# Optimization experiments

Measured on AMD Instinct MI355X. Metric: run time of the kernel, lower is better.

Reference implementation:

```python
import jax, jax.numpy as jnp
import numpy as np

S, B, V, E, H, L = 500, 64, 50257, 512, 512, 2


def setup_inputs() -> dict:
    key = jax.random.key(0)
    ks = jax.random.split(key, 12)
    u = lambda k, shape, s: jax.random.uniform(k, shape, jnp.float32, -s, s)
    kstd = 1.0 / np.sqrt(H)
    return {
        "inputs": jax.random.randint(ks[0], (S, B), 0, V, dtype=jnp.int64),
        "text_lengths": jax.random.randint(ks[1], (B,), 1, S, dtype=jnp.int64),
        "embedding": jax.random.normal(ks[2], (V, E), jnp.float32),
        "W_ih": u(ks[3], (4 * H, E), kstd),   # PyTorch LSTM gate order: i,f,g,o
        "W_hh": u(ks[4], (4 * H, H), kstd),
        "b_ih": u(ks[5], (4 * H,), kstd),
        "b_hh": u(ks[6], (4 * H,), kstd),
        "W_word": u(ks[7], (H, H), 0.1),
        "b_word": jnp.zeros((H, 1), jnp.float32),
        "w_proj": u(ks[8], (H, 1), 0.1),
        "dec_W": u(ks[9], (L, H), kstd),
        "dec_b": u(ks[10], (L,), kstd),
    }


def _lstm(x, W_ih, W_hh, b_ih, b_hh):
    # x: [S, B, E] -> states [S, B, H]
    Bsz = x.shape[1]
    Hn = W_hh.shape[1]
    # precompute input projections for all timesteps in one GEMM
    xproj = jnp.einsum('sbe,ge->sbg', x, W_ih) + b_ih + b_hh  # [S, B, 4H]

    def step(carry, xp):
        h, c = carry
        z = xp + h @ W_hh.T  # [B, 4H]
        i, f, g, o = jnp.split(z, 4, axis=-1)
        i, f, o = jax.nn.sigmoid(i), jax.nn.sigmoid(f), jax.nn.sigmoid(o)
        c = f * c + i * jnp.tanh(g)
        h = o * jnp.tanh(c)
        return (h, c), h

    h0 = jnp.zeros((Bsz, Hn), x.dtype)
    _, hs = jax.lax.scan(step, (h0, h0), xproj)
    return hs  # [S, B, H]


def reference(inputs, text_lengths, embedding, W_ih, W_hh, b_ih, b_hh,
              W_word, b_word, w_proj, dec_W, dec_b):
    # eval mode: dropout is identity
    embedded = embedding[inputs]                       # [S, B, E]
    states = _lstm(embedded, W_ih, W_hh, b_ih, b_hh)   # [S, B, H]
    # batch_matmul_bias with tanh: tanh(states @ W_word + b_word^T)
    word_squish = jnp.tanh(jnp.einsum('sbh,hk->sbk', states, W_word) + b_word[:, 0])
    # batch_matmul: project to scalar score per (s, b)
    word_attn = jnp.einsum('sbh,hk->sbk', word_squish, w_proj)[..., 0]  # [S, B]
    # softmax over sequence dim (nn.Softmax on [B, S] -> dim=1)
    attn = jax.nn.softmax(word_attn.T, axis=1).T       # [S, B]
    # attention_mul: weighted sum over S, keepdim -> [1, B, H]
    pooled = jnp.einsum('sb,sbh->bh', attn, states)[None]
    return pooled @ dec_W.T + dec_b                    # [1, B, labels]
```

## Files before the change

### kernel.cpp

```cpp
#include <hip/hip_runtime.h>


#define S_LEN 500
#define BATCH 64
#define EDIM 512
#define HDIM 512
#define TEAMS 8
#define WGS_PER_TEAM 32
#define TB 8
#define NBLOCKS (TEAMS * WGS_PER_TEAM)
#define NTHREADS 512

typedef unsigned long long ull;

#define XPROJ_BYTES  ((size_t)S_LEN * 2048 * BATCH * 4)
#define STATES_OFF   XPROJ_BYTES
#define STATES_BYTES ((size_t)S_LEN * BATCH * HDIM * 4)
#define HBUF_OFF     (STATES_OFF + STATES_BYTES)
#define HBUF_BYTES   ((size_t)2 * TEAMS * TB * HDIM * 8)
#define PART_OFF     (HBUF_OFF + HBUF_BYTES)
#define PART_BYTES   (4 * S_LEN * BATCH * 4)

__global__ __launch_bounds__(256) void xproj_gemm(
    const int* __restrict__ idx, const float* __restrict__ emb,
    const float* __restrict__ W_ih, const float* __restrict__ b_ih,
    const float* __restrict__ b_hh, float* __restrict__ xproj) {
  __shared__ float At[16][132];
  __shared__ float Bt[16][132];
  __shared__ int sidx[128];

  const int tid = threadIdx.x;
  const int sb0 = blockIdx.x * 128;
  const int g0  = blockIdx.y * 128;
  if (tid < 128) sidx[tid] = idx[sb0 + tid];

  const int ty = tid >> 4, tx = tid & 15;
  const int ra = tid & 127, pp = tid >> 7;

  float acc[8][8];
#pragma unroll
  for (int i = 0; i < 8; ++i)
#pragma unroll
    for (int j = 0; j < 8; ++j) acc[i][j] = 0.f;

  __syncthreads();

  for (int k0 = 0; k0 < 512; k0 += 16) {
    const float* pa = &W_ih[(size_t)(g0 + ra) * 512 + k0 + 8 * pp];
    float4 a0 = *(const float4*)pa, a1 = *(const float4*)(pa + 4);
    const float* pb = &emb[(size_t)sidx[ra] * 512 + k0 + 8 * pp];
    float4 b0 = *(const float4*)pb, b1 = *(const float4*)(pb + 4);
    At[8*pp+0][ra]=a0.x; At[8*pp+1][ra]=a0.y; At[8*pp+2][ra]=a0.z; At[8*pp+3][ra]=a0.w;
    At[8*pp+4][ra]=a1.x; At[8*pp+5][ra]=a1.y; At[8*pp+6][ra]=a1.z; At[8*pp+7][ra]=a1.w;
    Bt[8*pp+0][ra]=b0.x; Bt[8*pp+1][ra]=b0.y; Bt[8*pp+2][ra]=b0.z; Bt[8*pp+3][ra]=b0.w;
    Bt[8*pp+4][ra]=b1.x; Bt[8*pp+5][ra]=b1.y; Bt[8*pp+6][ra]=b1.z; Bt[8*pp+7][ra]=b1.w;
    __syncthreads();
#pragma unroll
    for (int kk = 0; kk < 16; ++kk) {
      float4 x0 = *(const float4*)&At[kk][ty * 8];
      float4 x1 = *(const float4*)&At[kk][ty * 8 + 4];
      float4 y0 = *(const float4*)&Bt[kk][tx * 8];
      float4 y1 = *(const float4*)&Bt[kk][tx * 8 + 4];
      float av[8] = {x0.x, x0.y, x0.z, x0.w, x1.x, x1.y, x1.z, x1.w};
      float bv[8] = {y0.x, y0.y, y0.z, y0.w, y1.x, y1.y, y1.z, y1.w};
#pragma unroll
      for (int i = 0; i < 8; ++i)
#pragma unroll
        for (int j = 0; j < 8; ++j) acc[i][j] = fmaf(av[i], bv[j], acc[i][j]);
    }
    __syncthreads();
  }
  const int sbb = sb0 + tx * 8;
  const int s  = sbb >> 6;
  const int tm = (sbb & 63) >> 3;
#pragma unroll
  for (int i = 0; i < 8; ++i) {
    const int g = g0 + ty * 8 + i;
    const float bias = b_ih[g] + b_hh[g];
    float* dst = &xproj[(((size_t)s * TEAMS + tm) * 2048 + g) * 8];
    float4 v0 = {acc[i][0] + bias, acc[i][1] + bias, acc[i][2] + bias, acc[i][3] + bias};
    float4 v1 = {acc[i][4] + bias, acc[i][5] + bias, acc[i][6] + bias, acc[i][7] + bias};
    *(float4*)dst = v0;
    *(float4*)(dst + 4) = v1;
  }
}

__global__ __launch_bounds__(NTHREADS, 1) void lstm_persistent(
    const float* __restrict__ xproj, const float* __restrict__ W_hh,
    float* __restrict__ states, ull* __restrict__ h_buf) {
  __shared__ float red[2][8][4][65];

  const int team = blockIdx.x & 7;
  const int wg   = blockIdx.x >> 3;
  const int tid  = threadIdx.x;
  const int wv   = tid >> 6;
  const int l    = tid & 63;

  const int g = 16 * wg + (l & 15) + 512 * (l >> 4);

  float whh[64];
  {
    const float4* phh = (const float4*)(W_hh + (size_t)g * HDIM + (size_t)wv * 64);
#pragma unroll
    for (int j = 0; j < 16; ++j) {
      float4 v = phh[j];
      whh[4*j+0] = v.x; whh[4*j+1] = v.y; whh[4*j+2] = v.z; whh[4*j+3] = v.w;
    }
  }

  const int gu = l & 15, gbl = l >> 4;
  const int unit = 16 * wg + gu;
  float c_state = 0.f;
  const float* xpbase = xproj + (size_t)(16 * wg + gu) * 8 + (wv * 4 + gbl);

  for (int s = 0; s < S_LEN; ++s) {
    const int par = s & 1, par2 = (s + 1) & 1;
#pragma unroll
    for (int G = 0; G < 2; ++G) {
      float xv0, xv1, xv2, xv3;
      if (wv == G) {
        const float* p = xpbase + ((size_t)s * TEAMS + team) * (2048 * 8);
        xv0 = p[0]; xv1 = p[512 * 8]; xv2 = p[1024 * 8]; xv3 = p[1536 * 8];
      }

      float acc0 = 0.f, acc1 = 0.f, acc2 = 0.f, acc3 = 0.f;
      if (s > 0) {
        const ull* hb = h_buf + (((size_t)par * TEAMS + team) * TB + G * 4) * HDIM
                        + (size_t)64 * wv + l;
        ull r0, r1, r2, r3;
        int spins = 0;
        for (;;) {
          r0 = __hip_atomic_load(hb + 0 * HDIM, __ATOMIC_RELAXED, __HIP_MEMORY_SCOPE_AGENT);
          r1 = __hip_atomic_load(hb + 1 * HDIM, __ATOMIC_RELAXED, __HIP_MEMORY_SCOPE_AGENT);
          r2 = __hip_atomic_load(hb + 2 * HDIM, __ATOMIC_RELAXED, __HIP_MEMORY_SCOPE_AGENT);
          r3 = __hip_atomic_load(hb + 3 * HDIM, __ATOMIC_RELAXED, __HIP_MEMORY_SCOPE_AGENT);
          bool ok = ((int)(r0 >> 32) == s) & ((int)(r1 >> 32) == s) &
                    ((int)(r2 >> 32) == s) & ((int)(r3 >> 32) == s);
          if (__all(ok)) break;
          __builtin_amdgcn_s_sleep(1);
          if (++spins > (1 << 18)) break;
        }
        const int h0 = (int)(unsigned)r0, h1 = (int)(unsigned)r1;
        const int h2 = (int)(unsigned)r2, h3 = (int)(unsigned)r3;
#pragma unroll
        for (int k = 0; k < 64; ++k) {
          const float wk = whh[k];
          acc0 = fmaf(wk, __int_as_float(__builtin_amdgcn_readlane(h0, k)), acc0);
          acc1 = fmaf(wk, __int_as_float(__builtin_amdgcn_readlane(h1, k)), acc1);
          acc2 = fmaf(wk, __int_as_float(__builtin_amdgcn_readlane(h2, k)), acc2);
          acc3 = fmaf(wk, __int_as_float(__builtin_amdgcn_readlane(h3, k)), acc3);
        }
      }

      red[G][wv][0][l] = acc0;
      red[G][wv][1][l] = acc1;
      red[G][wv][2][l] = acc2;
      red[G][wv][3][l] = acc3;
      __syncthreads();

      if (wv == G) {
        float z0 = xv0, z1 = xv1, z2 = xv2, z3 = xv3;
#pragma unroll
        for (int w2 = 0; w2 < 8; ++w2) {
          z0 += red[G][w2][gbl][gu +  0];
          z1 += red[G][w2][gbl][gu + 16];
          z2 += red[G][w2][gbl][gu + 32];
          z3 += red[G][w2][gbl][gu + 48];
        }
        float i_ = 1.f / (1.f + expf(-z0));
        float f_ = 1.f / (1.f + expf(-z1));
        float g_ = tanhf(z2);
        float o_ = 1.f / (1.f + expf(-z3));
        c_state = f_ * c_state + i_ * g_;
        float h_ = o_ * tanhf(c_state);
        ull pv = ((ull)(unsigned)(s + 1) << 32) | __float_as_uint(h_);
        __hip_atomic_store(
            &h_buf[(((size_t)par2 * TEAMS + team) * TB + G * 4 + gbl) * HDIM + unit],
            pv, __ATOMIC_RELAXED, __HIP_MEMORY_SCOPE_AGENT);
        states[((size_t)s * BATCH + team * TB + G * 4 + gbl) * HDIM + unit] = h_;
      }
    }
  }
}

#define ATP 132
__global__ __launch_bounds__(256) void attn_gemm(
    const float* __restrict__ states, const float* __restrict__ W_word,
    const float* __restrict__ b_word, const float* __restrict__ w_proj,
    float* __restrict__ part) {
  __shared__ float At[16][ATP];
  __shared__ float Bt[16][ATP];
  __shared__ float redl[128][17];

  const int tid = threadIdx.x;
  const int m0 = blockIdx.x * 128;
  const int n0 = blockIdx.y * 128;
  const int ty = tid >> 4, tx = tid & 15;

  float acc[8][8];
#pragma unroll
  for (int i = 0; i < 8; ++i)
#pragma unroll
    for (int j = 0; j < 8; ++j) acc[i][j] = 0.f;

  for (int k0 = 0; k0 < 512; k0 += 16) {
#pragma unroll
    for (int it = 0; it < 2; ++it) {
      int m = (tid >> 2) + 64 * it;
      int kq = tid & 3;
      float4 v = *(const float4*)&states[(size_t)(m0 + m) * 512 + k0 + 4 * kq];
      At[4 * kq + 0][m] = v.x; At[4 * kq + 1][m] = v.y;
      At[4 * kq + 2][m] = v.z; At[4 * kq + 3][m] = v.w;
    }
#pragma unroll
    for (int it = 0; it < 2; ++it) {
      int kr = (tid >> 5) + 8 * it;
      int nq = tid & 31;
      float4 v = *(const float4*)&W_word[(size_t)(k0 + kr) * 512 + n0 + 4 * nq];
      *(float4*)&Bt[kr][4 * nq] = v;
    }
    __syncthreads();
#pragma unroll
    for (int kk = 0; kk < 16; ++kk) {
      float4 a0 = *(const float4*)&At[kk][ty * 8];
      float4 a1 = *(const float4*)&At[kk][ty * 8 + 4];
      float4 b0 = *(const float4*)&Bt[kk][tx * 8];
      float4 b1 = *(const float4*)&Bt[kk][tx * 8 + 4];
      float av[8] = {a0.x, a0.y, a0.z, a0.w, a1.x, a1.y, a1.z, a1.w};
      float bv[8] = {b0.x, b0.y, b0.z, b0.w, b1.x, b1.y, b1.z, b1.w};
#pragma unroll
      for (int i = 0; i < 8; ++i)
#pragma unroll
        for (int j = 0; j < 8; ++j) acc[i][j] = fmaf(av[i], bv[j], acc[i][j]);
    }
    __syncthreads();
  }
  float bw[8], wp[8];
  {
    float4 v0 = *(const float4*)&b_word[n0 + tx * 8];
    float4 v1 = *(const float4*)&b_word[n0 + tx * 8 + 4];
    bw[0]=v0.x; bw[1]=v0.y; bw[2]=v0.z; bw[3]=v0.w; bw[4]=v1.x; bw[5]=v1.y; bw[6]=v1.z; bw[7]=v1.w;
    float4 u0 = *(const float4*)&w_proj[n0 + tx * 8];
    float4 u1 = *(const float4*)&w_proj[n0 + tx * 8 + 4];
    wp[0]=u0.x; wp[1]=u0.y; wp[2]=u0.z; wp[3]=u0.w; wp[4]=u1.x; wp[5]=u1.y; wp[6]=u1.z; wp[7]=u1.w;
  }
#pragma unroll
  for (int i = 0; i < 8; ++i) {
    float rs = 0.f;
#pragma unroll
    for (int j = 0; j < 8; ++j) rs += tanhf(acc[i][j] + bw[j]) * wp[j];
    redl[ty * 8 + i][tx] = rs;
  }
  __syncthreads();
  if (tid < 128) {
    float ssum = 0.f;
#pragma unroll
    for (int x = 0; x < 16; ++x) ssum += redl[tid][x];
    part[(size_t)blockIdx.y * (S_LEN * BATCH) + m0 + tid] = ssum;
  }
}

__global__ __launch_bounds__(256) void softmax_pool_decode(
    const float* __restrict__ part, const float* __restrict__ states,
    const float* __restrict__ dec_W, const float* __restrict__ dec_b,
    float* __restrict__ out) {
  const int b = blockIdx.x;
  const int tid = threadIdx.x;
  __shared__ float sc[S_LEN];
  __shared__ float pool[HDIM];
  __shared__ float redm[256];

  for (int s = tid; s < S_LEN; s += 256) {
    int t = s * BATCH + b;
    sc[s] = part[t] + part[S_LEN * BATCH + t] + part[2 * S_LEN * BATCH + t] +
            part[3 * S_LEN * BATCH + t];
  }
  __syncthreads();
  float m = -1e30f;
  for (int s = tid; s < S_LEN; s += 256) m = fmaxf(m, sc[s]);
  redm[tid] = m; __syncthreads();
  for (int o = 128; o > 0; o >>= 1) {
    if (tid < o) redm[tid] = fmaxf(redm[tid], redm[tid + o]);
    __syncthreads();
  }
  const float gmax = redm[0];
  __syncthreads();
  float lsum = 0.f;
  for (int s = tid; s < S_LEN; s += 256) { float e = expf(sc[s] - gmax); sc[s] = e; lsum += e; }
  redm[tid] = lsum; __syncthreads();
  for (int o = 128; o > 0; o >>= 1) {
    if (tid < o) redm[tid] += redm[tid + o];
    __syncthreads();
  }
  const float inv = 1.f / redm[0];
  __syncthreads();
  for (int h = tid; h < HDIM; h += 256) {
    float a = 0.f;
    for (int s = 0; s < S_LEN; ++s)
      a = fmaf(sc[s], states[((size_t)s * BATCH + b) * HDIM + h], a);
    pool[h] = a * inv;
  }
  __syncthreads();
  const int lcls = tid >> 7, ch = tid & 127;
  float p = 0.f;
#pragma unroll
  for (int j = 0; j < 4; ++j)
    p = fmaf(pool[ch * 4 + j], dec_W[lcls * HDIM + ch * 4 + j], p);
  redm[tid] = p; __syncthreads();
  for (int o = 64; o > 0; o >>= 1) {
    if (ch < o) redm[tid] += redm[tid + o];
    __syncthreads();
  }
  if (ch == 0) out[b * 2 + lcls] = redm[tid] + dec_b[lcls];
}

extern "C" void kernel_launch(void* const* d_in, const int* in_sizes, int n_in,
                              void* d_out, int out_size, void* d_ws, size_t ws_size,
                              hipStream_t stream) {
  const int*   idx    = (const int*)d_in[0];
  const float* emb    = (const float*)d_in[2];
  const float* W_ih   = (const float*)d_in[3];
  const float* W_hh   = (const float*)d_in[4];
  const float* b_ih   = (const float*)d_in[5];
  const float* b_hh   = (const float*)d_in[6];
  const float* W_word = (const float*)d_in[7];
  const float* b_word = (const float*)d_in[8];
  const float* w_proj = (const float*)d_in[9];
  const float* dec_W  = (const float*)d_in[10];
  const float* dec_b  = (const float*)d_in[11];
  float* out = (float*)d_out;

  char* ws = (char*)d_ws;
  float* xproj  = (float*)ws;
  float* states = (float*)(ws + STATES_OFF);
  ull*   h_buf  = (ull*)(ws + HBUF_OFF);
  float* part   = (float*)(ws + PART_OFF);

  hipMemsetAsync(h_buf, 0, HBUF_BYTES, stream);

  xproj_gemm<<<dim3(250, 16), 256, 0, stream>>>(idx, emb, W_ih, b_ih, b_hh, xproj);

  void* args[] = {(void*)&xproj, (void*)&W_hh, (void*)&states, (void*)&h_buf};
  hipLaunchCooperativeKernel(lstm_persistent, dim3(NBLOCKS), dim3(NTHREADS), args, 0, stream);

  attn_gemm<<<dim3(250, 4), 256, 0, stream>>>(states, W_word, b_word, w_proj, part);
  softmax_pool_decode<<<64, 256, 0, stream>>>(part, states, dec_W, dec_b, out);
}
```

Baseline: 3.123 ms.

## Merge LSTM half-batch passes into one step with single barrier and relayout xproj

The persistent LSTM kernel used to handle its 8 batch rows in two halves of 4 per timestep, each half with its own spin-wait, reduction and __syncthreads. It now waits once for all 8 rows, accumulates 8 dot products per lane, and needs one barrier per step. The 16 gate lanes of every wave each finalize one batch row, so all 8 waves share the nonlinear stage. The xproj GEMM epilogue writes a [s][team][b][gate] layout so gate lanes read contiguous values. The trade-off is more registers for the extra accumulators and hidden-state loads, a shared reduction buffer double-buffered on step parity, and a halved spin-timeout limit.

```diff
diff --git a/kernel.cpp b/kernel.cpp
--- a/kernel.cpp
+++ b/kernel.cpp
@@ -70,16 +70,20 @@
     }
     __syncthreads();
   }
+  float biasv[8];
+#pragma unroll
+  for (int i = 0; i < 8; ++i)
+    biasv[i] = b_ih[g0 + ty * 8 + i] + b_hh[g0 + ty * 8 + i];
   const int sbb = sb0 + tx * 8;
   const int s  = sbb >> 6;
   const int tm = (sbb & 63) >> 3;
 #pragma unroll
-  for (int i = 0; i < 8; ++i) {
-    const int g = g0 + ty * 8 + i;
-    const float bias = b_ih[g] + b_hh[g];
-    float* dst = &xproj[(((size_t)s * TEAMS + tm) * 2048 + g) * 8];
-    float4 v0 = {acc[i][0] + bias, acc[i][1] + bias, acc[i][2] + bias, acc[i][3] + bias};
-    float4 v1 = {acc[i][4] + bias, acc[i][5] + bias, acc[i][6] + bias, acc[i][7] + bias};
+  for (int j = 0; j < 8; ++j) {
+    float* dst = &xproj[(((size_t)s * TEAMS + tm) * TB + j) * 2048 + g0 + ty * 8];
+    float4 v0 = {acc[0][j] + biasv[0], acc[1][j] + biasv[1],
+                 acc[2][j] + biasv[2], acc[3][j] + biasv[3]};
+    float4 v1 = {acc[4][j] + biasv[4], acc[5][j] + biasv[5],
+                 acc[6][j] + biasv[6], acc[7][j] + biasv[7]};
     *(float4*)dst = v0;
     *(float4*)(dst + 4) = v1;
   }
@@ -88,7 +92,7 @@
 __global__ __launch_bounds__(NTHREADS, 1) void lstm_persistent(
     const float* __restrict__ xproj, const float* __restrict__ W_hh,
     float* __restrict__ states, ull* __restrict__ h_buf) {
-  __shared__ float red[2][8][4][65];
+  __shared__ float red[2][8][8][64];
 
   const int team = blockIdx.x & 7;
   const int wg   = blockIdx.x >> 3;
@@ -108,77 +112,96 @@
     }
   }
 
-  const int gu = l & 15, gbl = l >> 4;
+  const int gu = l & 15;
   const int unit = 16 * wg + gu;
+  const bool gate_lane = (l < 16);
   float c_state = 0.f;
-  const float* xpbase = xproj + (size_t)(16 * wg + gu) * 8 + (wv * 4 + gbl);
 
   for (int s = 0; s < S_LEN; ++s) {
     const int par = s & 1, par2 = (s + 1) & 1;
-#pragma unroll
-    for (int G = 0; G < 2; ++G) {
-      float xv0, xv1, xv2, xv3;
-      if (wv == G) {
-        const float* p = xpbase + ((size_t)s * TEAMS + team) * (2048 * 8);
-        xv0 = p[0]; xv1 = p[512 * 8]; xv2 = p[1024 * 8]; xv3 = p[1536 * 8];
+
+    float xv0, xv1, xv2, xv3;
+    if (gate_lane) {
+      const float* p = xproj + (((size_t)s * TEAMS + team) * TB + wv) * 2048;
+      xv0 = p[unit];
+      xv1 = p[unit + 512];
+      xv2 = p[unit + 1024];
+      xv3 = p[unit + 1536];
+    }
+
+    float a0 = 0.f, a1 = 0.f, a2 = 0.f, a3 = 0.f;
+    float a4 = 0.f, a5 = 0.f, a6 = 0.f, a7 = 0.f;
+
+    if (s > 0) {
+      const ull* hb = h_buf + (((size_t)par * TEAMS + team) * TB) * HDIM
+                      + (size_t)64 * wv + l;
+      ull r0, r1, r2, r3, r4, r5, r6, r7;
+      int spins = 0;
+      for (;;) {
+        r0 = __hip_atomic_load(hb + 0 * HDIM, __ATOMIC_RELAXED, __HIP_MEMORY_SCOPE_AGENT);
+        r1 = __hip_atomic_load(hb + 1 * HDIM, __ATOMIC_RELAXED, __HIP_MEMORY_SCOPE_AGENT);
+        r2 = __hip_atomic_load(hb + 2 * HDIM, __ATOMIC_RELAXED, __HIP_MEMORY_SCOPE_AGENT);
+        r3 = __hip_atomic_load(hb + 3 * HDIM, __ATOMIC_RELAXED, __HIP_MEMORY_SCOPE_AGENT);
+        r4 = __hip_atomic_load(hb + 4 * HDIM, __ATOMIC_RELAXED, __HIP_MEMORY_SCOPE_AGENT);
+        r5 = __hip_atomic_load(hb + 5 * HDIM, __ATOMIC_RELAXED, __HIP_MEMORY_SCOPE_AGENT);
+        r6 = __hip_atomic_load(hb + 6 * HDIM, __ATOMIC_RELAXED, __HIP_MEMORY_SCOPE_AGENT);
+        r7 = __hip_atomic_load(hb + 7 * HDIM, __ATOMIC_RELAXED, __HIP_MEMORY_SCOPE_AGENT);
+        bool ok = ((int)(r0 >> 32) == s) & ((int)(r1 >> 32) == s) &
+                  ((int)(r2 >> 32) == s) & ((int)(r3 >> 32) == s) &
+                  ((int)(r4 >> 32) == s) & ((int)(r5 >> 32) == s) &
+                  ((int)(r6 >> 32) == s) & ((int)(r7 >> 32) == s);
+        if (__all(ok)) break;
+        __builtin_amdgcn_s_sleep(1);
+        if (++spins > (1 << 17)) break;
       }
-
-      float acc0 = 0.f, acc1 = 0.f, acc2 = 0.f, acc3 = 0.f;
-      if (s > 0) {
-        const ull* hb = h_buf + (((size_t)par * TEAMS + team) * TB + G * 4) * HDIM
-                        + (size_t)64 * wv + l;
-        ull r0, r1, r2, r3;
-        int spins = 0;
-        for (;;) {
-          r0 = __hip_atomic_load(hb + 0 * HDIM, __ATOMIC_RELAXED, __HIP_MEMORY_SCOPE_AGENT);
-          r1 = __hip_atomic_load(hb + 1 * HDIM, __ATOMIC_RELAXED, __HIP_MEMORY_SCOPE_AGENT);
-          r2 = __hip_atomic_load(hb + 2 * HDIM, __ATOMIC_RELAXED, __HIP_MEMORY_SCOPE_AGENT);
-          r3 = __hip_atomic_load(hb + 3 * HDIM, __ATOMIC_RELAXED, __HIP_MEMORY_SCOPE_AGENT);
-          bool ok = ((int)(r0 >> 32) == s) & ((int)(r1 >> 32) == s) &
-                    ((int)(r2 >> 32) == s) & ((int)(r3 >> 32) == s);
-          if (__all(ok)) break;
-          __builtin_amdgcn_s_sleep(1);
-          if (++spins > (1 << 18)) break;
-        }
-        const int h0 = (int)(unsigned)r0, h1 = (int)(unsigned)r1;
-        const int h2 = (int)(unsigned)r2, h3 = (int)(unsigned)r3;
-#pragma unroll
-        for (int k = 0; k < 64; ++k) {
-          const float wk = whh[k];
-          acc0 = fmaf(wk, __int_as_float(__builtin_amdgcn_readlane(h0, k)), acc0);
-          acc1 = fmaf(wk, __int_as_float(__builtin_amdgcn_readlane(h1, k)), acc1);
-          acc2 = fmaf(wk, __int_as_float(__builtin_amdgcn_readlane(h2, k)), acc2);
-          acc3 = fmaf(wk, __int_as_float(__builtin_amdgcn_readlane(h3, k)), acc3);
-        }
+      const int h0 = (int)(unsigned)r0, h1 = (int)(unsigned)r1;
+      const int h2 = (int)(unsigned)r2, h3 = (int)(unsigned)r3;
+      const int h4 = (int)(unsigned)r4, h5 = (int)(unsigned)r5;
+      const int h6 = (int)(unsigned)r6, h7 = (int)(unsigned)r7;
+#pragma unroll
+      for (int k = 0; k < 64; ++k) {
+        const float wk = whh[k];
+        a0 = fmaf(wk, __int_as_float(__builtin_amdgcn_readlane(h0, k)), a0);
+        a1 = fmaf(wk, __int_as_float(__builtin_amdgcn_readlane(h1, k)), a1);
+        a2 = fmaf(wk, __int_as_float(__builtin_amdgcn_readlane(h2, k)), a2);
+        a3 = fmaf(wk, __int_as_float(__builtin_amdgcn_readlane(h3, k)), a3);
+        a4 = fmaf(wk, __int_as_float(__builtin_amdgcn_readlane(h4, k)), a4);
+        a5 = fmaf(wk, __int_as_float(__builtin_amdgcn_readlane(h5, k)), a5);
+        a6 = fmaf(wk, __int_as_float(__builtin_amdgcn_readlane(h6, k)), a6);
+        a7 = fmaf(wk, __int_as_float(__builtin_amdgcn_readlane(h7, k)), a7);
       }
-
-      red[G][wv][0][l] = acc0;
-      red[G][wv][1][l] = acc1;
-      red[G][wv][2][l] = acc2;
-      red[G][wv][3][l] = acc3;
-      __syncthreads();
-
-      if (wv == G) {
-        float z0 = xv0, z1 = xv1, z2 = xv2, z3 = xv3;
-#pragma unroll
-        for (int w2 = 0; w2 < 8; ++w2) {
-          z0 += red[G][w2][gbl][gu +  0];
-          z1 += red[G][w2][gbl][gu + 16];
-          z2 += red[G][w2][gbl][gu + 32];
-          z3 += red[G][w2][gbl][gu + 48];
-        }
-        float i_ = 1.f / (1.f + expf(-z0));
-        float f_ = 1.f / (1.f + expf(-z1));
-        float g_ = tanhf(z2);
-        float o_ = 1.f / (1.f + expf(-z3));
-        c_state = f_ * c_state + i_ * g_;
-        float h_ = o_ * tanhf(c_state);
-        ull pv = ((ull)(unsigned)(s + 1) << 32) | __float_as_uint(h_);
-        __hip_atomic_store(
-            &h_buf[(((size_t)par2 * TEAMS + team) * TB + G * 4 + gbl) * HDIM + unit],
-            pv, __ATOMIC_RELAXED, __HIP_MEMORY_SCOPE_AGENT);
-        states[((size_t)s * BATCH + team * TB + G * 4 + gbl) * HDIM + unit] = h_;
+    }
+
+    red[par][wv][0][l] = a0;
+    red[par][wv][1][l] = a1;
+    red[par][wv][2][l] = a2;
+    red[par][wv][3][l] = a3;
+    red[par][wv][4][l] = a4;
+    red[par][wv][5][l] = a5;
+    red[par][wv][6][l] = a6;
+    red[par][wv][7][l] = a7;
+    __syncthreads();
+
+    if (gate_lane) {
+      float z0 = xv0, z1 = xv1, z2 = xv2, z3 = xv3;
+#pragma unroll
+      for (int w2 = 0; w2 < 8; ++w2) {
+        z0 += red[par][w2][wv][gu +  0];
+        z1 += red[par][w2][wv][gu + 16];
+        z2 += red[par][w2][wv][gu + 32];
+        z3 += red[par][w2][wv][gu + 48];
       }
+      float i_ = 1.f / (1.f + expf(-z0));
+      float f_ = 1.f / (1.f + expf(-z1));
+      float g_ = tanhf(z2);
+      float o_ = 1.f / (1.f + expf(-z3));
+      c_state = f_ * c_state + i_ * g_;
+      float h_ = o_ * tanhf(c_state);
+      ull pv = ((ull)(unsigned)(s + 1) << 32) | __float_as_uint(h_);
+      __hip_atomic_store(
+          &h_buf[(((size_t)par2 * TEAMS + team) * TB + wv) * HDIM + unit],
+          pv, __ATOMIC_RELAXED, __HIP_MEMORY_SCOPE_AGENT);
+      states[((size_t)s * BATCH + team * TB + wv) * HDIM + unit] = h_;
     }
   }
 }
```

New measurement: 4.365 ms. 1.4x slower.

## Fuse input projection into persistent LSTM via producer warps computing next-step xproj

Applied to the files above, without the earlier changes.

Removes the separate xproj GEMM kernel and its large global buffer. Each persistent block is doubled to 1024 threads: 8 waves keep the recurrent loop and run at raised priority, while 8 extra waves hold W_ih slices in registers and compute the next timestep's input projection from gathered embedding rows. That projection is handed over through a double-buffered shared-memory array. This trades a big GEMM plus a global memory round-trip for work overlapped with the latency-bound recurrence, at the cost of more register pressure, shared barriers on the critical path, and less efficient readlane-based FMA for the projection.

```diff
diff --git a/kernel.cpp b/kernel.cpp
--- a/kernel.cpp
+++ b/kernel.cpp
@@ -6,178 +6,164 @@
 #define EDIM 512
 #define HDIM 512
 #define TEAMS 8
-#define WGS_PER_TEAM 32
 #define TB 8
-#define NBLOCKS (TEAMS * WGS_PER_TEAM)
-#define NTHREADS 512
+#define NTHREADS 1024
+#define NBLOCKS 256
 
 typedef unsigned long long ull;
 
-#define XPROJ_BYTES  ((size_t)S_LEN * 2048 * BATCH * 4)
-#define STATES_OFF   XPROJ_BYTES
 #define STATES_BYTES ((size_t)S_LEN * BATCH * HDIM * 4)
-#define HBUF_OFF     (STATES_OFF + STATES_BYTES)
+#define HBUF_OFF     STATES_BYTES
 #define HBUF_BYTES   ((size_t)2 * TEAMS * TB * HDIM * 8)
 #define PART_OFF     (HBUF_OFF + HBUF_BYTES)
 #define PART_BYTES   (4 * S_LEN * BATCH * 4)
 
-__global__ __launch_bounds__(256) void xproj_gemm(
+__global__ __launch_bounds__(NTHREADS, 4) void fused_lstm(
     const int* __restrict__ idx, const float* __restrict__ emb,
     const float* __restrict__ W_ih, const float* __restrict__ b_ih,
-    const float* __restrict__ b_hh, float* __restrict__ xproj) {
-  __shared__ float At[16][132];
-  __shared__ float Bt[16][132];
-  __shared__ int sidx[128];
-
-  const int tid = threadIdx.x;
-  const int sb0 = blockIdx.x * 128;
-  const int g0  = blockIdx.y * 128;
-  if (tid < 128) sidx[tid] = idx[sb0 + tid];
-
-  const int ty = tid >> 4, tx = tid & 15;
-  const int ra = tid & 127, pp = tid >> 7;
-
-  float acc[8][8];
-#pragma unroll
-  for (int i = 0; i < 8; ++i)
-#pragma unroll
-    for (int j = 0; j < 8; ++j) acc[i][j] = 0.f;
-
-  __syncthreads();
-
-  for (int k0 = 0; k0 < 512; k0 += 16) {
-    const float* pa = &W_ih[(size_t)(g0 + ra) * 512 + k0 + 8 * pp];
-    float4 a0 = *(const float4*)pa, a1 = *(const float4*)(pa + 4);
-    const float* pb = &emb[(size_t)sidx[ra] * 512 + k0 + 8 * pp];
-    float4 b0 = *(const float4*)pb, b1 = *(const float4*)(pb + 4);
-    At[8*pp+0][ra]=a0.x; At[8*pp+1][ra]=a0.y; At[8*pp+2][ra]=a0.z; At[8*pp+3][ra]=a0.w;
-    At[8*pp+4][ra]=a1.x; At[8*pp+5][ra]=a1.y; At[8*pp+6][ra]=a1.z; At[8*pp+7][ra]=a1.w;
-    Bt[8*pp+0][ra]=b0.x; Bt[8*pp+1][ra]=b0.y; Bt[8*pp+2][ra]=b0.z; Bt[8*pp+3][ra]=b0.w;
-    Bt[8*pp+4][ra]=b1.x; Bt[8*pp+5][ra]=b1.y; Bt[8*pp+6][ra]=b1.z; Bt[8*pp+7][ra]=b1.w;
-    __syncthreads();
-#pragma unroll
-    for (int kk = 0; kk < 16; ++kk) {
-      float4 x0 = *(const float4*)&At[kk][ty * 8];
-      float4 x1 = *(const float4*)&At[kk][ty * 8 + 4];
-      float4 y0 = *(const float4*)&Bt[kk][tx * 8];
-      float4 y1 = *(const float4*)&Bt[kk][tx * 8 + 4];
-      float av[8] = {x0.x, x0.y, x0.z, x0.w, x1.x, x1.y, x1.z, x1.w};
-      float bv[8] = {y0.x, y0.y, y0.z, y0.w, y1.x, y1.y, y1.z, y1.w};
-#pragma unroll
-      for (int i = 0; i < 8; ++i)
-#pragma unroll
-        for (int j = 0; j < 8; ++j) acc[i][j] = fmaf(av[i], bv[j], acc[i][j]);
-    }
-    __syncthreads();
-  }
-  const int sbb = sb0 + tx * 8;
-  const int s  = sbb >> 6;
-  const int tm = (sbb & 63) >> 3;
-#pragma unroll
-  for (int i = 0; i < 8; ++i) {
-    const int g = g0 + ty * 8 + i;
-    const float bias = b_ih[g] + b_hh[g];
-    float* dst = &xproj[(((size_t)s * TEAMS + tm) * 2048 + g) * 8];
-    float4 v0 = {acc[i][0] + bias, acc[i][1] + bias, acc[i][2] + bias, acc[i][3] + bias};
-    float4 v1 = {acc[i][4] + bias, acc[i][5] + bias, acc[i][6] + bias, acc[i][7] + bias};
-    *(float4*)dst = v0;
-    *(float4*)(dst + 4) = v1;
-  }
-}
-
-__global__ __launch_bounds__(NTHREADS, 1) void lstm_persistent(
-    const float* __restrict__ xproj, const float* __restrict__ W_hh,
+    const float* __restrict__ b_hh, const float* __restrict__ W_hh,
     float* __restrict__ states, ull* __restrict__ h_buf) {
   __shared__ float red[2][8][4][65];
-
+  __shared__ float red2[2][8][4][64];
+  __shared__ float xpF[2][8][72];
+
+  const int tid  = threadIdx.x;
   const int team = blockIdx.x & 7;
   const int wg   = blockIdx.x >> 3;
-  const int tid  = threadIdx.x;
-  const int wv   = tid >> 6;
+  const int lw   = tid >> 6;
   const int l    = tid & 63;
 
   const int g = 16 * wg + (l & 15) + 512 * (l >> 4);
 
-  float whh[64];
-  {
-    const float4* phh = (const float4*)(W_hh + (size_t)g * HDIM + (size_t)wv * 64);
-#pragma unroll
-    for (int j = 0; j < 16; ++j) {
-      float4 v = phh[j];
-      whh[4*j+0] = v.x; whh[4*j+1] = v.y; whh[4*j+2] = v.z; whh[4*j+3] = v.w;
-    }
-  }
-
-  const int gu = l & 15, gbl = l >> 4;
-  const int unit = 16 * wg + gu;
-  float c_state = 0.f;
-  const float* xpbase = xproj + (size_t)(16 * wg + gu) * 8 + (wv * 4 + gbl);
-
-  for (int s = 0; s < S_LEN; ++s) {
-    const int par = s & 1, par2 = (s + 1) & 1;
-#pragma unroll
-    for (int G = 0; G < 2; ++G) {
-      float xv0, xv1, xv2, xv3;
-      if (wv == G) {
-        const float* p = xpbase + ((size_t)s * TEAMS + team) * (2048 * 8);
-        xv0 = p[0]; xv1 = p[512 * 8]; xv2 = p[1024 * 8]; xv3 = p[1536 * 8];
+  if (lw < 8) {
+    __builtin_amdgcn_s_setprio(1);
+    const int wv = lw;
+    float whh[64];
+    {
+      const float4* phh = (const float4*)(W_hh + (size_t)g * HDIM + (size_t)wv * 64);
+#pragma unroll
+      for (int j = 0; j < 16; ++j) {
+        float4 v = phh[j];
+        whh[4*j+0] = v.x; whh[4*j+1] = v.y; whh[4*j+2] = v.z; whh[4*j+3] = v.w;
       }
-
-      float acc0 = 0.f, acc1 = 0.f, acc2 = 0.f, acc3 = 0.f;
-      if (s > 0) {
-        const ull* hb = h_buf + (((size_t)par * TEAMS + team) * TB + G * 4) * HDIM
-                        + (size_t)64 * wv + l;
-        ull r0, r1, r2, r3;
-        int spins = 0;
-        for (;;) {
-          r0 = __hip_atomic_load(hb + 0 * HDIM, __ATOMIC_RELAXED, __HIP_MEMORY_SCOPE_AGENT);
-          r1 = __hip_atomic_load(hb + 1 * HDIM, __ATOMIC_RELAXED, __HIP_MEMORY_SCOPE_AGENT);
-          r2 = __hip_atomic_load(hb + 2 * HDIM, __ATOMIC_RELAXED, __HIP_MEMORY_SCOPE_AGENT);
-          r3 = __hip_atomic_load(hb + 3 * HDIM, __ATOMIC_RELAXED, __HIP_MEMORY_SCOPE_AGENT);
-          bool ok = ((int)(r0 >> 32) == s) & ((int)(r1 >> 32) == s) &
-                    ((int)(r2 >> 32) == s) & ((int)(r3 >> 32) == s);
-          if (__all(ok)) break;
-          __builtin_amdgcn_s_sleep(1);
-          if (++spins > (1 << 18)) break;
-        }
-        const int h0 = (int)(unsigned)r0, h1 = (int)(unsigned)r1;
-        const int h2 = (int)(unsigned)r2, h3 = (int)(unsigned)r3;
-#pragma unroll
-        for (int k = 0; k < 64; ++k) {
-          const float wk = whh[k];
-          acc0 = fmaf(wk, __int_as_float(__builtin_amdgcn_readlane(h0, k)), acc0);
-          acc1 = fmaf(wk, __int_as_float(__builtin_amdgcn_readlane(h1, k)), acc1);
-          acc2 = fmaf(wk, __int_as_float(__builtin_amdgcn_readlane(h2, k)), acc2);
-          acc3 = fmaf(wk, __int_as_float(__builtin_amdgcn_readlane(h3, k)), acc3);
+    }
+    const int gu = l & 15, gbl = l >> 4;
+    const int unit = 16 * wg + gu;
+    float c_state = 0.f;
+
+    for (int s = -1; s < S_LEN; ++s) {
+      const int par = s & 1, par2 = (s + 1) & 1;
+#pragma unroll
+      for (int G = 0; G < 2; ++G) {
+        float acc0 = 0.f, acc1 = 0.f, acc2 = 0.f, acc3 = 0.f;
+        if (s > 0) {
+          const ull* hb = h_buf + (((size_t)par * TEAMS + team) * TB + G * 4) * HDIM
+                          + (size_t)64 * wv + l;
+          ull r0, r1, r2, r3;
+          int spins = 0;
+          for (;;) {
+            r0 = __hip_atomic_load(hb + 0 * HDIM, __ATOMIC_RELAXED, __HIP_MEMORY_SCOPE_AGENT);
+            r1 = __hip_atomic_load(hb + 1 * HDIM, __ATOMIC_RELAXED, __HIP_MEMORY_SCOPE_AGENT);
+            r2 = __hip_atomic_load(hb + 2 * HDIM, __ATOMIC_RELAXED, __HIP_MEMORY_SCOPE_AGENT);
+            r3 = __hip_atomic_load(hb + 3 * HDIM, __ATOMIC_RELAXED, __HIP_MEMORY_SCOPE_AGENT);
+            bool ok = ((int)(r0 >> 32) == s) & ((int)(r1 >> 32) == s) &
+                      ((int)(r2 >> 32) == s) & ((int)(r3 >> 32) == s);
+            if (__all(ok)) break;
+            __builtin_amdgcn_s_sleep(1);
+            if (++spins > (1 << 18)) break;
+          }
+          const int h0 = (int)(unsigned)r0, h1 = (int)(unsigned)r1;
+          const int h2 = (int)(unsigned)r2, h3 = (int)(unsigned)r3;
+#pragma unroll
+          for (int k = 0; k < 64; ++k) {
+            const float wk = whh[k];
+            acc0 = fmaf(wk, __int_as_float(__builtin_amdgcn_readlane(h0, k)), acc0);
+            acc1 = fmaf(wk, __int_as_float(__builtin_amdgcn_readlane(h1, k)), acc1);
+            acc2 = fmaf(wk, __int_as_float(__builtin_amdgcn_readlane(h2, k)), acc2);
+            acc3 = fmaf(wk, __int_as_float(__builtin_amdgcn_readlane(h3, k)), acc3);
+          }
+        }
+        if (s >= 0) {
+          red[G][wv][0][l] = acc0;
+          red[G][wv][1][l] = acc1;
+          red[G][wv][2][l] = acc2;
+          red[G][wv][3][l] = acc3;
+        }
+        __syncthreads();
+        if (s >= 0 && wv == G) {
+          float z0 = xpF[par][G * 4 + gbl][gu +  0];
+          float z1 = xpF[par][G * 4 + gbl][gu + 16];
+          float z2 = xpF[par][G * 4 + gbl][gu + 32];
+          float z3 = xpF[par][G * 4 + gbl][gu + 48];
+#pragma unroll
+          for (int w2 = 0; w2 < 8; ++w2) {
+            z0 += red[G][w2][gbl][gu +  0];
+            z1 += red[G][w2][gbl][gu + 16];
+            z2 += red[G][w2][gbl][gu + 32];
+            z3 += red[G][w2][gbl][gu + 48];
+          }
+          float i_ = 1.f / (1.f + expf(-z0));
+          float f_ = 1.f / (1.f + expf(-z1));
+          float g_ = tanhf(z2);
+          float o_ = 1.f / (1.f + expf(-z3));
+          c_state = f_ * c_state + i_ * g_;
+          float h_ = o_ * tanhf(c_state);
+          ull pv = ((ull)(unsigned)(s + 1) << 32) | __float_as_uint(h_);
+          __hip_atomic_store(
+              &h_buf[(((size_t)par2 * TEAMS + team) * TB + G * 4 + gbl) * HDIM + unit],
+              pv, __ATOMIC_RELAXED, __HIP_MEMORY_SCOPE_AGENT);
+          states[((size_t)s * BATCH + team * TB + G * 4 + gbl) * HDIM + unit] = h_;
         }
       }
-
-      red[G][wv][0][l] = acc0;
-      red[G][wv][1][l] = acc1;
-      red[G][wv][2][l] = acc2;
-      red[G][wv][3][l] = acc3;
-      __syncthreads();
-
-      if (wv == G) {
-        float z0 = xv0, z1 = xv1, z2 = xv2, z3 = xv3;
-#pragma unroll
-        for (int w2 = 0; w2 < 8; ++w2) {
-          z0 += red[G][w2][gbl][gu +  0];
-          z1 += red[G][w2][gbl][gu + 16];
-          z2 += red[G][w2][gbl][gu + 32];
-          z3 += red[G][w2][gbl][gu + 48];
-        }
-        float i_ = 1.f / (1.f + expf(-z0));
-        float f_ = 1.f / (1.f + expf(-z1));
-        float g_ = tanhf(z2);
-        float o_ = 1.f / (1.f + expf(-z3));
-        c_state = f_ * c_state + i_ * g_;
-        float h_ = o_ * tanhf(c_state);
-        ull pv = ((ull)(unsigned)(s + 1) << 32) | __float_as_uint(h_);
-        __hip_atomic_store(
-            &h_buf[(((size_t)par2 * TEAMS + team) * TB + G * 4 + gbl) * HDIM + unit],
-            pv, __ATOMIC_RELAXED, __HIP_MEMORY_SCOPE_AGENT);
-        states[((size_t)s * BATCH + team * TB + G * 4 + gbl) * HDIM + unit] = h_;
+    }
+  } else {
+    const int pw = lw - 8;
+    float wih[64];
+    {
+      const float4* pih = (const float4*)(W_ih + (size_t)g * EDIM + (size_t)pw * 64);
+#pragma unroll
+      for (int j = 0; j < 16; ++j) {
+        float4 v = pih[j];
+        wih[4*j+0] = v.x; wih[4*j+1] = v.y; wih[4*j+2] = v.z; wih[4*j+3] = v.w;
+      }
+    }
+    const float bias = b_ih[g] + b_hh[g];
+
+    for (int s = -1; s < S_LEN; ++s) {
+#pragma unroll
+      for (int G = 0; G < 2; ++G) {
+        const int sp = s + 1;
+        if (sp < S_LEN) {
+          const int b0 = team * TB + G * 4;
+          const int r0i = idx[sp * BATCH + b0 + 0];
+          const int r1i = idx[sp * BATCH + b0 + 1];
+          const int r2i = idx[sp * BATCH + b0 + 2];
+          const int r3i = idx[sp * BATCH + b0 + 3];
+          const int e0 = __float_as_int(emb[(size_t)r0i * EDIM + 64 * pw + l]);
+          const int e1 = __float_as_int(emb[(size_t)r1i * EDIM + 64 * pw + l]);
+          const int e2 = __float_as_int(emb[(size_t)r2i * EDIM + 64 * pw + l]);
+          const int e3 = __float_as_int(emb[(size_t)r3i * EDIM + 64 * pw + l]);
+          float a0 = 0.f, a1 = 0.f, a2 = 0.f, a3 = 0.f;
+#pragma unroll
+          for (int k = 0; k < 64; ++k) {
+            const float wk = wih[k];
+            a0 = fmaf(wk, __int_as_float(__builtin_amdgcn_readlane(e0, k)), a0);
+            a1 = fmaf(wk, __int_as_float(__builtin_amdgcn_readlane(e1, k)), a1);
+            a2 = fmaf(wk, __int_as_float(__builtin_amdgcn_readlane(e2, k)), a2);
+            a3 = fmaf(wk, __int_as_float(__builtin_amdgcn_readlane(e3, k)), a3);
+          }
+          red2[G][pw][0][l] = a0;
+          red2[G][pw][1][l] = a1;
+          red2[G][pw][2][l] = a2;
+          red2[G][pw][3][l] = a3;
+        }
+        __syncthreads();
+        if (sp < S_LEN && pw < 4) {
+          float z = bias;
+#pragma unroll
+          for (int c = 0; c < 8; ++c) z += red2[G][c][pw][l];
+          xpF[sp & 1][G * 4 + pw][l] = z;
+        }
       }
     }
   }
@@ -331,17 +317,15 @@
   float* out = (float*)d_out;
 
   char* ws = (char*)d_ws;
-  float* xproj  = (float*)ws;
-  float* states = (float*)(ws + STATES_OFF);
+  float* states = (float*)ws;
   ull*   h_buf  = (ull*)(ws + HBUF_OFF);
   float* part   = (float*)(ws + PART_OFF);
 
   hipMemsetAsync(h_buf, 0, HBUF_BYTES, stream);
 
-  xproj_gemm<<<dim3(250, 16), 256, 0, stream>>>(idx, emb, W_ih, b_ih, b_hh, xproj);
-
-  void* args[] = {(void*)&xproj, (void*)&W_hh, (void*)&states, (void*)&h_buf};
-  hipLaunchCooperativeKernel(lstm_persistent, dim3(NBLOCKS), dim3(NTHREADS), args, 0, stream);
+  void* args[] = {(void*)&idx, (void*)&emb, (void*)&W_ih, (void*)&b_ih,
+                  (void*)&b_hh, (void*)&W_hh, (void*)&states, (void*)&h_buf};
+  hipLaunchCooperativeKernel(fused_lstm, dim3(NBLOCKS), dim3(NTHREADS), args, 0, stream);
 
   attn_gemm<<<dim3(250, 4), 256, 0, stream>>>(states, W_word, b_word, w_proj, part);
   softmax_pool_decode<<<64, 256, 0, stream>>>(part, states, dec_W, dec_b, out);
```

New measurement: 5.908 ms. +89.2%, slower.
